# Kernel optimization log

Measured on AMD Instinct MI355X. Metric: run time of the kernel, lower is better.

The kernel has to match this reference:

```python
import jax, jax.numpy as jnp
import numpy as np

D = 1024
HEADS = 16
HD = D // HEADS


def setup_inputs() -> dict:
    key = jax.random.key(0)
    kx, kqkv, kout = jax.random.split(key, 3)
    x = jax.random.normal(kx, (2, 2048, D), dtype=jnp.float32)
    # torch Linear weight is [out, in]; store same layout
    W_qkv = jax.random.normal(kqkv, (3 * D, D), dtype=jnp.float32) * (D ** -0.5)
    W_out = jax.random.normal(kout, (D, D), dtype=jnp.float32) * (D ** -0.5)
    return {"x": x, "W_qkv": W_qkv, "W_out": W_out}


def reference(x, W_qkv, W_out):
    B, T, _ = x.shape
    scale = HD ** -0.5
    qkv = jnp.einsum('btd,ed->bte', x, W_qkv)            # [B,T,3D]
    qkv = qkv.reshape(B, T, 3, HEADS, HD)
    q = jnp.transpose(qkv[:, :, 0], (0, 2, 1, 3))        # [B,H,T,hd]
    k = jnp.transpose(qkv[:, :, 1], (0, 2, 1, 3))
    v = jnp.transpose(qkv[:, :, 2], (0, 2, 1, 3))
    attn = jnp.einsum('bhqd,bhkd->bhqk', q, k) * scale   # [B,H,T,T]
    causal = jnp.tril(jnp.ones((T, T), dtype=bool))
    attn = jnp.where(causal, attn, -jnp.inf)
    attn = jax.nn.softmax(attn, axis=-1)
    out = jnp.einsum('bhqk,bhkd->bhqd', attn, v)         # [B,H,T,hd]
    out = jnp.transpose(out, (0, 2, 1, 3)).reshape(B, T, HEADS * HD)
    return jnp.einsum('btd,ed->bte', out, W_out)
```

## Files before the change

### kernel.cpp

```cpp
#include <hip/hip_runtime.h>
#include <cmath>


typedef unsigned short u16;
typedef unsigned int u32;
typedef short short8 __attribute__((ext_vector_type(8)));
typedef float floatx4 __attribute__((ext_vector_type(4)));

#define T_SZ 2048
#define HD_SZ 64
#define QSCALE 0.1803368801111244f

__device__ __forceinline__ u16 f2bf(float f) {
  unsigned u = __float_as_uint(f);
  u += 0x7fffu + ((u >> 16) & 1u);
  return (u16)(u >> 16);
}

__device__ __forceinline__ u32 pack_bf2(float lo, float hi) {
  return __builtin_amdgcn_perm(__float_as_uint(hi), __float_as_uint(lo), 0x07060302u);
}

__device__ __forceinline__ u32 cvtpk(float a, float b) {
  u32 r;
  asm("v_cvt_pk_bf16_f32 %0, %1, %2" : "=v"(r) : "v"(a), "v"(b));
  return r;
}

__device__ __forceinline__ void pl32swap(u32& a, u32& b) {
  asm("v_permlane32_swap_b32 %0, %1" : "+v"(a), "+v"(b));
}
__device__ __forceinline__ void pl16swap(u32& a, u32& b) {
  asm("v_permlane16_swap_b32 %0, %1" : "+v"(a), "+v"(b));
}

__device__ __forceinline__ void gload16(const u16* g, u16* l) {
  __builtin_amdgcn_global_load_lds(
      (const __attribute__((address_space(1))) void*)g,
      (__attribute__((address_space(3))) void*)l, 16, 0, 0);
}

__global__ __launch_bounds__(256) void cast3(const float* __restrict__ a, u16* __restrict__ ao, int na4,
                                             const float* __restrict__ b, u16* __restrict__ bo, int nb4,
                                             const float* __restrict__ c, u16* __restrict__ co, int nc4) {
  int i = blockIdx.x * 256 + threadIdx.x;
  const float* src;
  u16* dst;
  int j;
  if (i < na4) { src = a; dst = ao; j = i; }
  else if (i < na4 + nb4) { src = b; dst = bo; j = i - na4; }
  else { j = i - na4 - nb4; if (j >= nc4) return; src = c; dst = co; }
  float4 f = ((const float4*)src)[j];
  ushort4 o;
  o.x = f2bf(f.x); o.y = f2bf(f.y); o.z = f2bf(f.z); o.w = f2bf(f.w);
  ((ushort4*)dst)[j] = o;
}

__global__ __launch_bounds__(256, 3) void gemm_qkv(const u16* __restrict__ A,
                                                   const u16* __restrict__ Bt,
                                                   u16* __restrict__ Qf,
                                                   u16* __restrict__ Kf,
                                                   u16* __restrict__ Vf) {
  __shared__ u16 SM[2 * 128 * 64];
  u16* As = SM;
  u16* Bs = SM + 128 * 64;
  const int Kdim = 1024;
  const int tid = threadIdx.x;
  const int lane = tid & 63;
  const int wave = tid >> 6;
  const int quad = lane >> 4;
  const int l16 = lane & 15;
  const int wm = wave >> 1, wn = wave & 1;
  const int m0 = blockIdx.y * 128;
  const int n0 = blockIdx.x * 128;

  floatx4 acc[4][4];
#pragma unroll
  for (int i = 0; i < 4; i++)
#pragma unroll
    for (int j = 0; j < 4; j++) acc[i][j] = (floatx4){0.f, 0.f, 0.f, 0.f};

  const int srow = lane >> 3;
  const int scol = ((lane & 7) ^ srow) * 8;
  const u16* gpA[4];
  const u16* gpB[4];
  u16 *lpA[4], *lpB[4];
#pragma unroll
  for (int u = 0; u < 4; u++) {
    const int row = wave * 32 + u * 8 + srow;
    gpA[u] = A + (size_t)(m0 + row) * Kdim + scol;
    gpB[u] = Bt + (size_t)(n0 + row) * Kdim + scol;
    lpA[u] = As + (wave * 32 + u * 8) * 64 + lane * 8;
    lpB[u] = Bs + (wave * 32 + u * 8) * 64 + lane * 8;
  }

  const int fsw = l16 & 7;

  for (int k0 = 0; k0 < Kdim; k0 += 64) {
    __syncthreads();
#pragma unroll
    for (int u = 0; u < 4; u++) {
      gload16(gpA[u] + k0, lpA[u]);
      gload16(gpB[u] + k0, lpB[u]);
    }
    __syncthreads();

#pragma unroll
    for (int h = 0; h < 2; h++) {
      const int seg = ((h * 4 + quad) ^ fsw) * 8;
      short8 af[4], bf[4];
#pragma unroll
      for (int mt = 0; mt < 4; mt++)
        af[mt] = *(const short8*)&As[(wm * 64 + mt * 16 + l16) * 64 + seg];
#pragma unroll
      for (int nt = 0; nt < 4; nt++)
        bf[nt] = *(const short8*)&Bs[(wn * 64 + nt * 16 + l16) * 64 + seg];
#pragma unroll
      for (int mt = 0; mt < 4; mt++)
#pragma unroll
        for (int nt = 0; nt < 4; nt++)
          acc[mt][nt] = __builtin_amdgcn_mfma_f32_16x16x32_bf16(af[mt], bf[nt], acc[mt][nt], 0, 0, 0);
    }
  }

  const int dest = n0 >> 10;
  const int n0w = n0 + wn * 64;
  const int m_abs = m0 + wm * 64;
  const int b = m_abs >> 11;
  const int t0w = m_abs & 2047;
  const int h = (n0w >> 6) & 15;
  const int bh = b * 16 + h;
  u16* dstp = (dest == 0) ? Qf : (dest == 1) ? Kf : Vf;

  auto do_epi = [&](u16* ep) {
    if (dest == 2) {
#pragma unroll
      for (int nt = 0; nt < 4; nt++) {
#pragma unroll
        for (int mt = 0; mt < 4; mt++) {
          uint2 w;
          w.x = (u32)f2bf(acc[mt][nt][0]) | ((u32)f2bf(acc[mt][nt][1]) << 16);
          w.y = (u32)f2bf(acc[mt][nt][2]) | ((u32)f2bf(acc[mt][nt][3]) << 16);
          *(uint2*)&ep[(nt * 16 + l16) * 72 + mt * 16 + quad * 4] = w;
        }
      }
    } else {
      const float sc = (dest == 0) ? QSCALE : 1.0f;
#pragma unroll
      for (int mt = 0; mt < 4; mt++)
#pragma unroll
        for (int nt = 0; nt < 4; nt++)
#pragma unroll
          for (int r = 0; r < 4; r++)
            ep[(mt * 16 + quad * 4 + r) * 72 + nt * 16 + l16] =
                f2bf(acc[mt][nt][r] * sc);
    }
#pragma unroll
    for (int blk = 0; blk < 8; blk++) {
      const int tgd = blk >> 1;
      const int half = blk & 1;
      const short8 v = *(const short8*)&ep[(tgd * 16 + l16) * 72 + half * 32 + quad * 8];
      size_t base;
      if (dest == 0)
        base = ((size_t)(bh * 128 + (t0w >> 4) + tgd) * 2 + half) * 512;
      else
        base = (((size_t)(bh * 32 + (t0w >> 6)) * 4 + tgd) * 2 + half) * 512;
      *(short8*)(dstp + base + lane * 8) = v;
    }
  };

  __syncthreads();
  if (wave < 2) do_epi(&SM[wave * 64 * 72]);
  __syncthreads();
  if (wave >= 2) do_epi(&SM[(wave - 2) * 64 * 72]);
}

__global__ __launch_bounds__(256, 4) void gemm_out(const u16* __restrict__ A,
                                                   const u16* __restrict__ Bt,
                                                   float* __restrict__ Cout) {
  __shared__ u16 As[64 * 64];
  __shared__ u16 Bs[128 * 64];
  const int Kdim = 1024;
  const int tid = threadIdx.x;
  const int lane = tid & 63;
  const int wave = tid >> 6;
  const int quad = lane >> 4;
  const int l16 = lane & 15;
  const int wm = wave >> 1, wn = wave & 1;
  const int m0 = blockIdx.y * 64;
  const int n0 = blockIdx.x * 128;

  floatx4 acc[2][4];
#pragma unroll
  for (int i = 0; i < 2; i++)
#pragma unroll
    for (int j = 0; j < 4; j++) acc[i][j] = (floatx4){0.f, 0.f, 0.f, 0.f};

  const int srow = lane >> 3;
  const int scol = ((lane & 7) ^ srow) * 8;
  const u16* gpA[2];
  const u16* gpB[4];
  u16 *lpA[2], *lpB[4];
#pragma unroll
  for (int u = 0; u < 2; u++) {
    const int row = wave * 16 + u * 8 + srow;
    gpA[u] = A + (size_t)(m0 + row) * Kdim + scol;
    lpA[u] = As + (wave * 16 + u * 8) * 64 + lane * 8;
  }
#pragma unroll
  for (int u = 0; u < 4; u++) {
    const int row = wave * 32 + u * 8 + srow;
    gpB[u] = Bt + (size_t)(n0 + row) * Kdim + scol;
    lpB[u] = Bs + (wave * 32 + u * 8) * 64 + lane * 8;
  }

  const int fsw = l16 & 7;

  for (int k0 = 0; k0 < Kdim; k0 += 64) {
    __syncthreads();
#pragma unroll
    for (int u = 0; u < 2; u++) gload16(gpA[u] + k0, lpA[u]);
#pragma unroll
    for (int u = 0; u < 4; u++) gload16(gpB[u] + k0, lpB[u]);
    __syncthreads();

#pragma unroll
    for (int h = 0; h < 2; h++) {
      const int seg = ((h * 4 + quad) ^ fsw) * 8;
      short8 af[2], bf[4];
#pragma unroll
      for (int mt = 0; mt < 2; mt++)
        af[mt] = *(const short8*)&As[(wm * 32 + mt * 16 + l16) * 64 + seg];
#pragma unroll
      for (int nt = 0; nt < 4; nt++)
        bf[nt] = *(const short8*)&Bs[(wn * 64 + nt * 16 + l16) * 64 + seg];
#pragma unroll
      for (int mt = 0; mt < 2; mt++)
#pragma unroll
        for (int nt = 0; nt < 4; nt++)
          acc[mt][nt] = __builtin_amdgcn_mfma_f32_16x16x32_bf16(af[mt], bf[nt], acc[mt][nt], 0, 0, 0);
    }
  }

#pragma unroll
  for (int mt = 0; mt < 2; mt++)
#pragma unroll
    for (int nt = 0; nt < 4; nt++)
#pragma unroll
      for (int r = 0; r < 4; r++) {
        const int m = m0 + wm * 32 + mt * 16 + quad * 4 + r;
        const int n = n0 + wn * 64 + nt * 16 + l16;
        Cout[(size_t)m * 1024 + n] = acc[mt][nt][r];
      }
}

__global__ __launch_bounds__(256, 2) void flash_attn(const u16* __restrict__ Qf,
                                                     const u16* __restrict__ Kf,
                                                     const u16* __restrict__ Vf,
                                                     u16* __restrict__ Og) {
  __shared__ __align__(16) u16 KV[2][16 * 512];
  const int tid = threadIdx.x;
  const int lane = tid & 63, wave = tid >> 6;
  const int quad = lane >> 4, l16 = lane & 15;
  const int bh = blockIdx.x;
  const int py = blockIdx.y;
  const int p = (py < 8) ? py : 23 - py;
  const int gA = p, gB = 31 - p;
  const int b = bh >> 4, h = bh & 15;
  const u16* Qb = Qf + ((size_t)bh << 17);
  const u16* Kb = Kf + ((size_t)bh << 17);
  const u16* Vb = Vf + ((size_t)bh << 17);

  const u16* qpA = Qb + ((size_t)(gA * 4 + wave)) * 1024 + lane * 8;
  const u16* qpB = Qb + ((size_t)(gB * 4 + wave)) * 1024 + lane * 8;
  const short8 qfA0 = *(const short8*)qpA;
  const short8 qfA1 = *(const short8*)(qpA + 512);
  const short8 qfB0 = *(const short8*)qpB;
  const short8 qfB1 = *(const short8*)(qpB + 512);

  float lA = 0.f, lB = 0.f;
  floatx4 oA[4], oB[4];
#pragma unroll
  for (int dt = 0; dt < 4; dt++) {
    oA[dt] = (floatx4){0.f, 0.f, 0.f, 0.f};
    oB[dt] = (floatx4){0.f, 0.f, 0.f, 0.f};
  }

  const u16* gkv[4];
  u16* l0[4];
  u16* l1[4];
#pragma unroll
  for (int i = 0; i < 4; i++) {
    const int c = wave * 4 + i;
    gkv[i] = ((c < 8) ? (Kb + c * 512) : (Vb + (c - 8) * 512)) + lane * 8;
    l0[i] = &KV[0][c * 512] + lane * 8;
    l1[i] = &KV[1][c * 512] + lane * 8;
  }

  auto load_tile = [&](int kt, u16* const* lp) {
#pragma unroll
    for (int i = 0; i < 4; i++) gload16(gkv[i] + (size_t)kt * 4096, lp[i]);
  };

  const floatx4 zero4 = {0.f, 0.f, 0.f, 0.f};

  auto stream_step = [&](const short8 (*ka)[2], const short8 (*va)[2], bool diag,
                         const short8& qf0, const short8& qf1,
                         floatx4* o_acc, float& l_sum) {
    floatx4 sacc[4];
#pragma unroll
    for (int nt = 0; nt < 4; nt++) {
      if (diag && nt > wave) continue;
      floatx4 s = __builtin_amdgcn_mfma_f32_16x16x32_bf16(ka[nt][0], qf0, zero4, 0, 0, 0);
      sacc[nt] = __builtin_amdgcn_mfma_f32_16x16x32_bf16(ka[nt][1], qf1, s, 0, 0, 0);
    }
    u32 c[4][2];
#pragma unroll
    for (int nt = 0; nt < 4; nt++) {
      float p0 = 0.f, p1 = 0.f, p2 = 0.f, p3 = 0.f;
      if (!(diag && nt > wave)) {
        p0 = exp2f(sacc[nt][0]);
        p1 = exp2f(sacc[nt][1]);
        p2 = exp2f(sacc[nt][2]);
        p3 = exp2f(sacc[nt][3]);
        if (diag && nt == wave) {
          if (quad * 4 + 0 > l16) p0 = 0.f;
          if (quad * 4 + 1 > l16) p1 = 0.f;
          if (quad * 4 + 2 > l16) p2 = 0.f;
          if (quad * 4 + 3 > l16) p3 = 0.f;
        }
        l_sum += (p0 + p1) + (p2 + p3);
      }
      c[nt][0] = cvtpk(p0, p1);
      c[nt][1] = cvtpk(p2, p3);
    }
    pl32swap(c[0][0], c[1][0]); pl16swap(c[0][0], c[1][0]);
    pl32swap(c[0][1], c[1][1]); pl16swap(c[0][1], c[1][1]);
    pl32swap(c[2][0], c[3][0]); pl16swap(c[2][0], c[3][0]);
    pl32swap(c[2][1], c[3][1]); pl16swap(c[2][1], c[3][1]);
    union { u32 w[4]; short8 s8; } P0, P1;
    P0.w[0] = c[0][0]; P0.w[1] = c[0][1]; P0.w[2] = c[1][0]; P0.w[3] = c[1][1];
    P1.w[0] = c[2][0]; P1.w[1] = c[2][1]; P1.w[2] = c[3][0]; P1.w[3] = c[3][1];
    const short8 pf0 = P0.s8;
    const short8 pf1 = P1.s8;
    const bool skip_hi = diag && (wave < 2);
#pragma unroll
    for (int dt = 0; dt < 4; dt++) {
      o_acc[dt] = __builtin_amdgcn_mfma_f32_16x16x32_bf16(va[dt][0], pf0, o_acc[dt], 0, 0, 0);
      if (!skip_hi)
        o_acc[dt] = __builtin_amdgcn_mfma_f32_16x16x32_bf16(va[dt][1], pf1, o_acc[dt], 0, 0, 0);
    }
  };

  auto compute = [&](int kt, const u16* Kl) {
    short8 ka[4][2], va[4][2];
#pragma unroll
    for (int nt = 0; nt < 4; nt++)
#pragma unroll
      for (int hh = 0; hh < 2; hh++)
        ka[nt][hh] = *(const short8*)&Kl[(nt * 2 + hh) * 512 + lane * 8];
#pragma unroll
    for (int dt = 0; dt < 4; dt++)
#pragma unroll
      for (int hh = 0; hh < 2; hh++)
        va[dt][hh] = *(const short8*)&Kl[4096 + (dt * 2 + hh) * 512 + lane * 8];
    stream_step(ka, va, kt == gB, qfB0, qfB1, oB, lB);
    if (kt <= gA) stream_step(ka, va, kt == gA, qfA0, qfA1, oA, lA);
  };

  load_tile(0, l0);
  __syncthreads();
  int kt = 0;
  for (;;) {
    if (kt < gB) load_tile(kt + 1, l1);
    compute(kt, &KV[0][0]);
    if (++kt > gB) break;
    __syncthreads();
    if (kt < gB) load_tile(kt + 1, l0);
    compute(kt, &KV[1][0]);
    if (++kt > gB) break;
    __syncthreads();
  }

  auto write_tile = [&](int g, floatx4* o_acc, float l_sum) {
    l_sum += __shfl_xor(l_sum, 16, 64);
    l_sum += __shfl_xor(l_sum, 32, 64);
    const float inv_l = 1.0f / l_sum;
    const int t0 = g * 64 + wave * 16;
    const size_t row = ((size_t)(b * 2048 + t0 + l16) << 10) + h * 64;
#pragma unroll
    for (int dt = 0; dt < 4; dt++) {
      uint2 w;
      w.x = pack_bf2(o_acc[dt][0] * inv_l, o_acc[dt][1] * inv_l);
      w.y = pack_bf2(o_acc[dt][2] * inv_l, o_acc[dt][3] * inv_l);
      *(uint2*)&Og[row + dt * 16 + quad * 4] = w;
    }
  };
  write_tile(gA, oA, lA);
  write_tile(gB, oB, lB);
}

extern "C" void kernel_launch(void* const* d_in, const int* in_sizes, int n_in,
                              void* d_out, int out_size, void* d_ws, size_t ws_size,
                              hipStream_t stream) {
  const float* x = (const float*)d_in[0];
  const float* Wqkv = (const float*)d_in[1];
  const float* Wout = (const float*)d_in[2];
  float* out = (float*)d_out;

  char* ws = (char*)d_ws;
  u16* xb    = (u16*)(ws + 0);
  u16* wqkvb = (u16*)(ws + 8388608);
  u16* woutb = (u16*)(ws + 14680064);
  u16* Qf    = (u16*)(ws + 16777216);
  u16* Kf    = (u16*)(ws + 25165824);
  u16* Vf    = (u16*)(ws + 33554432);
  u16* attn  = (u16*)(ws + 41943040);

  cast3<<<8192, 256, 0, stream>>>(x, xb, 1048576, Wqkv, wqkvb, 786432,
                                  Wout, woutb, 262144);

  gemm_qkv<<<dim3(24, 32), 256, 0, stream>>>(xb, wqkvb, Qf, Kf, Vf);

  flash_attn<<<dim3(32, 16), 256, 0, stream>>>(Qf, Kf, Vf, attn);

  gemm_out<<<dim3(8, 64), 256, 0, stream>>>(attn, woutb, out);
}
```

Measured before the change: 160.2 us.

## Split paired query tiles into one tile per block with higher occupancy

Each flash attention block now handles a single 64-row query tile instead of a paired light/heavy pair that shared KV loads, doubling the grid to 1024 blocks. The tile order interleaves short and long causal tiles across blockIdx.y. Launch bounds rise to 4 blocks per CU to cut register pressure, and V fragments are loaded after the softmax to shorten live ranges. The cost is that each KV tile is loaded from global and LDS separately for each query tile rather than once per pair, and per-block work becomes unbalanced.

```diff
diff --git a/kernel.cpp b/kernel.cpp
--- a/kernel.cpp
+++ b/kernel.cpp
@@ -254,7 +254,7 @@
       }
 }
 
-__global__ __launch_bounds__(256, 2) void flash_attn(const u16* __restrict__ Qf,
+__global__ __launch_bounds__(256, 4) void flash_attn(const u16* __restrict__ Qf,
                                                      const u16* __restrict__ Kf,
                                                      const u16* __restrict__ Vf,
                                                      u16* __restrict__ Og) {
@@ -263,28 +263,22 @@
   const int lane = tid & 63, wave = tid >> 6;
   const int quad = lane >> 4, l16 = lane & 15;
   const int bh = blockIdx.x;
-  const int py = blockIdx.y;
-  const int p = (py < 8) ? py : 23 - py;
-  const int gA = p, gB = 31 - p;
+  const int by = blockIdx.y;
+  const int r = by & 7, qq = by >> 3;
+  const int g = (qq == 0) ? r : (qq == 1) ? 15 - r : (qq == 2) ? 16 + r : 31 - r;
   const int b = bh >> 4, h = bh & 15;
   const u16* Qb = Qf + ((size_t)bh << 17);
   const u16* Kb = Kf + ((size_t)bh << 17);
   const u16* Vb = Vf + ((size_t)bh << 17);
 
-  const u16* qpA = Qb + ((size_t)(gA * 4 + wave)) * 1024 + lane * 8;
-  const u16* qpB = Qb + ((size_t)(gB * 4 + wave)) * 1024 + lane * 8;
-  const short8 qfA0 = *(const short8*)qpA;
-  const short8 qfA1 = *(const short8*)(qpA + 512);
-  const short8 qfB0 = *(const short8*)qpB;
-  const short8 qfB1 = *(const short8*)(qpB + 512);
-
-  float lA = 0.f, lB = 0.f;
-  floatx4 oA[4], oB[4];
-#pragma unroll
-  for (int dt = 0; dt < 4; dt++) {
-    oA[dt] = (floatx4){0.f, 0.f, 0.f, 0.f};
-    oB[dt] = (floatx4){0.f, 0.f, 0.f, 0.f};
-  }
+  const u16* qp = Qb + ((size_t)(g * 4 + wave)) * 1024 + lane * 8;
+  const short8 qf0 = *(const short8*)qp;
+  const short8 qf1 = *(const short8*)(qp + 512);
+
+  float l_sum = 0.f;
+  floatx4 o_acc[4];
+#pragma unroll
+  for (int dt = 0; dt < 4; dt++) o_acc[dt] = (floatx4){0.f, 0.f, 0.f, 0.f};
 
   const u16* gkv[4];
   u16* l0[4];
@@ -304,9 +298,14 @@
 
   const floatx4 zero4 = {0.f, 0.f, 0.f, 0.f};
 
-  auto stream_step = [&](const short8 (*ka)[2], const short8 (*va)[2], bool diag,
-                         const short8& qf0, const short8& qf1,
-                         floatx4* o_acc, float& l_sum) {
+  auto compute = [&](int kt, const u16* Kl) {
+    const bool diag = (kt == g);
+    short8 ka[4][2];
+#pragma unroll
+    for (int nt = 0; nt < 4; nt++)
+#pragma unroll
+      for (int hh = 0; hh < 2; hh++)
+        ka[nt][hh] = *(const short8*)&Kl[(nt * 2 + hh) * 512 + lane * 8];
     floatx4 sacc[4];
 #pragma unroll
     for (int nt = 0; nt < 4; nt++) {
@@ -343,6 +342,12 @@
     P1.w[0] = c[2][0]; P1.w[1] = c[2][1]; P1.w[2] = c[3][0]; P1.w[3] = c[3][1];
     const short8 pf0 = P0.s8;
     const short8 pf1 = P1.s8;
+    short8 va[4][2];
+#pragma unroll
+    for (int dt = 0; dt < 4; dt++)
+#pragma unroll
+      for (int hh = 0; hh < 2; hh++)
+        va[dt][hh] = *(const short8*)&Kl[4096 + (dt * 2 + hh) * 512 + lane * 8];
     const bool skip_hi = diag && (wave < 2);
 #pragma unroll
     for (int dt = 0; dt < 4; dt++) {
@@ -352,52 +357,32 @@
     }
   };
 
-  auto compute = [&](int kt, const u16* Kl) {
-    short8 ka[4][2], va[4][2];
-#pragma unroll
-    for (int nt = 0; nt < 4; nt++)
-#pragma unroll
-      for (int hh = 0; hh < 2; hh++)
-        ka[nt][hh] = *(const short8*)&Kl[(nt * 2 + hh) * 512 + lane * 8];
-#pragma unroll
-    for (int dt = 0; dt < 4; dt++)
-#pragma unroll
-      for (int hh = 0; hh < 2; hh++)
-        va[dt][hh] = *(const short8*)&Kl[4096 + (dt * 2 + hh) * 512 + lane * 8];
-    stream_step(ka, va, kt == gB, qfB0, qfB1, oB, lB);
-    if (kt <= gA) stream_step(ka, va, kt == gA, qfA0, qfA1, oA, lA);
-  };
-
   load_tile(0, l0);
   __syncthreads();
   int kt = 0;
   for (;;) {
-    if (kt < gB) load_tile(kt + 1, l1);
+    if (kt < g) load_tile(kt + 1, l1);
     compute(kt, &KV[0][0]);
-    if (++kt > gB) break;
-    __syncthreads();
-    if (kt < gB) load_tile(kt + 1, l0);
+    if (++kt > g) break;
+    __syncthreads();
+    if (kt < g) load_tile(kt + 1, l0);
     compute(kt, &KV[1][0]);
-    if (++kt > gB) break;
-    __syncthreads();
-  }
-
-  auto write_tile = [&](int g, floatx4* o_acc, float l_sum) {
-    l_sum += __shfl_xor(l_sum, 16, 64);
-    l_sum += __shfl_xor(l_sum, 32, 64);
-    const float inv_l = 1.0f / l_sum;
-    const int t0 = g * 64 + wave * 16;
-    const size_t row = ((size_t)(b * 2048 + t0 + l16) << 10) + h * 64;
-#pragma unroll
-    for (int dt = 0; dt < 4; dt++) {
-      uint2 w;
-      w.x = pack_bf2(o_acc[dt][0] * inv_l, o_acc[dt][1] * inv_l);
-      w.y = pack_bf2(o_acc[dt][2] * inv_l, o_acc[dt][3] * inv_l);
-      *(uint2*)&Og[row + dt * 16 + quad * 4] = w;
-    }
-  };
-  write_tile(gA, oA, lA);
-  write_tile(gB, oB, lB);
+    if (++kt > g) break;
+    __syncthreads();
+  }
+
+  l_sum += __shfl_xor(l_sum, 16, 64);
+  l_sum += __shfl_xor(l_sum, 32, 64);
+  const float inv_l = 1.0f / l_sum;
+  const int t0 = g * 64 + wave * 16;
+  const size_t row = ((size_t)(b * 2048 + t0 + l16) << 10) + h * 64;
+#pragma unroll
+  for (int dt = 0; dt < 4; dt++) {
+    uint2 w;
+    w.x = pack_bf2(o_acc[dt][0] * inv_l, o_acc[dt][1] * inv_l);
+    w.y = pack_bf2(o_acc[dt][2] * inv_l, o_acc[dt][3] * inv_l);
+    *(uint2*)&Og[row + dt * 16 + quad * 4] = w;
+  }
 }
 
 extern "C" void kernel_launch(void* const* d_in, const int* in_sizes, int n_in,
@@ -422,7 +407,7 @@
 
   gemm_qkv<<<dim3(24, 32), 256, 0, stream>>>(xb, wqkvb, Qf, Kf, Vf);
 
-  flash_attn<<<dim3(32, 16), 256, 0, stream>>>(Qf, Kf, Vf, attn);
+  flash_attn<<<dim3(32, 32), 256, 0, stream>>>(Qf, Kf, Vf, attn);
 
   gemm_out<<<dim3(8, 64), 256, 0, stream>>>(attn, woutb, out);
 }
```

Result: slower. 166.1 us (+3.7%).
